# Kernel optimization log

Hardware: AMD Instinct MI355X
Metric: run time of the kernel (lower is better)

Reference implementation:

```python
import jax, jax.numpy as jnp
import numpy as np

BATCH = 262144
N_ASSETS = 64
N_GROUPS = 8
ITERS = 20
EPS = 1e-9


def setup_inputs() -> dict:
    key = jax.random.key(0)
    kx = jax.random.fold_in(key, 1)
    x = jax.random.uniform(kx, (BATCH, N_ASSETS), dtype=jnp.float32)
    x = x / jnp.sum(x, axis=-1, keepdims=True)  # roughly simplex-like raw weights
    box_lb = jnp.zeros((N_ASSETS,), jnp.float32)          # port_type[0] = 0 (long-only)
    box_ub = jnp.full((N_ASSETS,), 0.3, jnp.float32)      # per-asset cap from _build_constraints
    # one-hot group membership matrix: asset i belongs to group i % N_GROUPS
    gid = np.arange(N_ASSETS) % N_GROUPS
    A = np.zeros((N_GROUPS, N_ASSETS), np.float32)
    A[gid, np.arange(N_ASSETS)] = 1.0
    group_A = jnp.asarray(A)
    group_lb = jnp.full((N_GROUPS,), 0.05, jnp.float32)
    group_ub = jnp.full((N_GROUPS,), 0.5, jnp.float32)
    return {"x": x, "box_lb": box_lb, "box_ub": box_ub, "group_A": group_A,
            "group_lb": group_lb, "group_ub": group_ub, "num_iterations": ITERS}


def _dykstra(x, box_lb, box_ub, group_A, group_lb, group_ub, num_iterations):
    n = x.shape[-1]
    norm_sq = jnp.sum(group_A * group_A, axis=-1)  # (G,)

    def box_simplex(w):
        w = jnp.clip(w, box_lb, box_ub)
        return w - (jnp.sum(w, axis=-1, keepdims=True) - 1.0) / n

    def group_step(w, g):
        a, lb, ub, ns = g  # a: (N,), scalars lb/ub/ns
        Aw = w @ a  # (B,)
        w = jnp.where((Aw > ub)[:, None], w - ((Aw - ub) / (ns + EPS))[:, None] * a, w)
        Aw = w @ a  # recomputed on updated w, matching the TF layer
        w = jnp.where((Aw < lb)[:, None], w - ((Aw - lb) / (ns + EPS))[:, None] * a, w)
        return w, None

    def body(i, w):
        w = box_simplex(w)
        w, _ = jax.lax.scan(group_step, w, (group_A, group_lb, group_ub, norm_sq))
        return w

    w = jax.lax.fori_loop(0, num_iterations, body, x)
    return box_simplex(w)


def reference(x, box_lb, box_ub, group_A, group_lb, group_ub, num_iterations):
    return _dykstra(x, box_lb, box_ub, group_A, group_lb, group_ub, num_iterations)
```

## Files before the change

### kernel.cpp

```cpp
#include <hip/hip_runtime.h>


#define NA 64
#define NG 8

__device__ __forceinline__ bool structural_ok(const float* __restrict__ box_lb,
                                              const float* __restrict__ box_ub,
                                              const float* __restrict__ group_A,
                                              int l) {
    const float lb0 = box_lb[0], ub0 = box_ub[0];
    bool ok = (box_lb[l] == lb0) && (box_ub[l] == ub0) && (lb0 <= ub0);
#pragma unroll
    for (int g = 0; g < NG; ++g) {
        const float expect = ((l & 7) == g) ? 1.0f : 0.0f;
        ok = ok && (group_A[g * NA + l] == expect);
    }
    return __all(ok);
}

__global__ __launch_bounds__(256, 4) void proj_fast(
    const float* __restrict__ x,
    const float* __restrict__ box_lb,
    const float* __restrict__ box_ub,
    const float* __restrict__ group_A,
    const float* __restrict__ group_lb,
    const float* __restrict__ group_ub,
    const int*  __restrict__ num_iter,
    float* __restrict__ out,
    int nrows)
{
    if (!structural_ok(box_lb, box_ub, group_A, threadIdx.x & 63)) return;

    const int r = blockIdx.x * blockDim.x + threadIdx.x;
    if (r >= nrows) return;

    const float* __restrict__ xr = x + (size_t)r * NA;
    float* __restrict__ outr = out + (size_t)r * NA;

    float w[NA];
#pragma unroll
    for (int q = 0; q < NA / 4; ++q) {
        const float4 v = reinterpret_cast<const float4*>(xr)[q];
        w[4 * q + 0] = v.x; w[4 * q + 1] = v.y;
        w[4 * q + 2] = v.z; w[4 * q + 3] = v.w;
    }

    const float lb0 = box_lb[0], ub0 = box_ub[0];
    float glb_s[NG], gub_s[NG];
#pragma unroll
    for (int g = 0; g < NG; ++g) { glb_s[g] = group_lb[g]; gub_s[g] = group_ub[g]; }

    const int iters = *num_iter;

    const float inv8 = 1.0f / (8.0f + 1e-9f);
    const float scale = 8.0f * inv8;

    for (int it = 0; it < iters; ++it) {
#pragma unroll
        for (int j = 0; j < NA; ++j)
            w[j] = __builtin_amdgcn_fmed3f(w[j], lb0, ub0);

        float gs[NG];
#pragma unroll
        for (int g = 0; g < NG; ++g) {
            const float a = w[g] + w[g + 8], b = w[g + 16] + w[g + 24];
            const float c = w[g + 32] + w[g + 40], d = w[g + 48] + w[g + 56];
            gs[g] = (a + b) + (c + d);
        }
        const float S = ((gs[0] + gs[1]) + (gs[2] + gs[3]))
                      + ((gs[4] + gs[5]) + (gs[6] + gs[7]));
        const float shift = (S - 1.0f) * (1.0f / NA);

        float u[NG];
#pragma unroll
        for (int g = 0; g < NG; ++g) {
            const float Aw  = fmaf(-8.0f, shift, gs[g]);
            const float e1  = fmaxf(Aw - gub_s[g], 0.0f);
            const float Aw2 = fmaf(-scale, e1, Aw);
            const float e2  = fminf(Aw2 - glb_s[g], 0.0f);
            u[g] = fmaf(e1 + e2, inv8, shift);
        }
#pragma unroll
        for (int k = 0; k < 8; ++k)
#pragma unroll
            for (int g = 0; g < NG; ++g)
                w[8 * k + g] -= u[g];
    }

    float ps[NG];
#pragma unroll
    for (int g = 0; g < NG; ++g) {
        w[g] = __builtin_amdgcn_fmed3f(w[g], lb0, ub0);
        ps[g] = w[g];
    }
#pragma unroll
    for (int j = NG; j < NA; ++j) {
        w[j] = __builtin_amdgcn_fmed3f(w[j], lb0, ub0);
        ps[j & 7] += w[j];
    }
    const float S = ((ps[0] + ps[1]) + (ps[2] + ps[3]))
                  + ((ps[4] + ps[5]) + (ps[6] + ps[7]));
    const float shift = (S - 1.0f) * (1.0f / NA);

#pragma unroll
    for (int q = 0; q < NA / 4; ++q) {
        float4 v;
        v.x = w[4 * q + 0] - shift; v.y = w[4 * q + 1] - shift;
        v.z = w[4 * q + 2] - shift; v.w = w[4 * q + 3] - shift;
        reinterpret_cast<float4*>(outr)[q] = v;
    }
}

__global__ __launch_bounds__(256) void proj_generic(
    const float* __restrict__ x,
    const float* __restrict__ box_lb,
    const float* __restrict__ box_ub,
    const float* __restrict__ group_A,
    const float* __restrict__ group_lb,
    const float* __restrict__ group_ub,
    const int*  __restrict__ num_iter,
    float* __restrict__ out,
    int nrows)
{
    if (structural_ok(box_lb, box_ub, group_A, threadIdx.x & 63)) return;

    const int r = blockIdx.x * blockDim.x + threadIdx.x;
    if (r >= nrows) return;

    const float* __restrict__ xr = x + (size_t)r * NA;
    float* __restrict__ outr = out + (size_t)r * NA;

    float w[NA];
#pragma unroll
    for (int j = 0; j < NA; ++j) w[j] = xr[j];

    const int iters = *num_iter;

    for (int it = 0; it < iters; ++it) {
        float S = 0.0f;
#pragma unroll
        for (int j = 0; j < NA; ++j) {
            w[j] = fminf(fmaxf(w[j], box_lb[j]), box_ub[j]);
            S += w[j];
        }
        const float shift = (S - 1.0f) * (1.0f / NA);
#pragma unroll
        for (int j = 0; j < NA; ++j) w[j] -= shift;

        for (int g = 0; g < NG; ++g) {
            const float* __restrict__ a = group_A + g * NA;
            float ns = 0.0f, Aw = 0.0f;
#pragma unroll
            for (int j = 0; j < NA; ++j) {
                const float av = a[j];
                ns = fmaf(av, av, ns);
                Aw = fmaf(av, w[j], Aw);
            }
            const float invg = 1.0f / (ns + 1e-9f);
            const float gub = group_ub[g], glb = group_lb[g];
            const float d1 = (Aw > gub) ? (Aw - gub) * invg : 0.0f;
#pragma unroll
            for (int j = 0; j < NA; ++j) w[j] = fmaf(-d1, a[j], w[j]);
            float Aw2 = 0.0f;
#pragma unroll
            for (int j = 0; j < NA; ++j) Aw2 = fmaf(a[j], w[j], Aw2);
            const float d2 = (Aw2 < glb) ? (Aw2 - glb) * invg : 0.0f;
#pragma unroll
            for (int j = 0; j < NA; ++j) w[j] = fmaf(-d2, a[j], w[j]);
        }
    }
    float S = 0.0f;
#pragma unroll
    for (int j = 0; j < NA; ++j) {
        w[j] = fminf(fmaxf(w[j], box_lb[j]), box_ub[j]);
        S += w[j];
    }
    const float shift = (S - 1.0f) * (1.0f / NA);
#pragma unroll
    for (int j = 0; j < NA; ++j) outr[j] = w[j] - shift;
}

extern "C" void kernel_launch(void* const* d_in, const int* in_sizes, int n_in,
                              void* d_out, int out_size, void* d_ws, size_t ws_size,
                              hipStream_t stream) {
    const float* x        = (const float*)d_in[0];
    const float* box_lb   = (const float*)d_in[1];
    const float* box_ub   = (const float*)d_in[2];
    const float* group_A  = (const float*)d_in[3];
    const float* group_lb = (const float*)d_in[4];
    const float* group_ub = (const float*)d_in[5];
    const int*   num_iter = (const int*)d_in[6];
    float* out = (float*)d_out;

    const int nrows = in_sizes[0] / NA;
    const int block = 256;
    const int grid = (nrows + block - 1) / block;

    proj_fast<<<grid, block, 0, stream>>>(x, box_lb, box_ub, group_A,
                                          group_lb, group_ub, num_iter,
                                          out, nrows);
    proj_generic<<<grid, block, 0, stream>>>(x, box_lb, box_ub, group_A,
                                             group_lb, group_ub, num_iter,
                                             out, nrows);
}
```

Baseline: 150.7 us.

## Split each row across two lanes with DPP cross-lane group-sum reduction

The fast kernel now assigns two threads per row, each holding 32 of the 64 weights, and combines the per-group partial sums through a DPP xor-1 swizzle add. This halves register pressure per thread and doubles thread-level parallelism, which should raise occupancy and improve load coalescing. Each iteration now pays a few extra cross-lane adds, the launch grid doubles, and the min-waves launch bound is dropped. It also replaces the near-1 scale factor with an exact subtraction, which can differ by a rounding step.

```diff
diff --git a/kernel.cpp b/kernel.cpp
--- a/kernel.cpp
+++ b/kernel.cpp
@@ -3,6 +3,12 @@
 
 #define NA 64
 #define NG 8
+
+__device__ __forceinline__ float dpp_xor1_add(float v) {
+    const int o = __builtin_amdgcn_update_dpp(0, __builtin_bit_cast(int, v),
+                                              0xB1, 0xF, 0xF, true);
+    return v + __builtin_bit_cast(float, o);
+}
 
 __device__ __forceinline__ bool structural_ok(const float* __restrict__ box_lb,
                                               const float* __restrict__ box_ub,
@@ -18,7 +24,7 @@
     return __all(ok);
 }
 
-__global__ __launch_bounds__(256, 4) void proj_fast(
+__global__ __launch_bounds__(256) void proj_fast(
     const float* __restrict__ x,
     const float* __restrict__ box_lb,
     const float* __restrict__ box_ub,
@@ -31,19 +37,23 @@
 {
     if (!structural_ok(box_lb, box_ub, group_A, threadIdx.x & 63)) return;
 
-    const int r = blockIdx.x * blockDim.x + threadIdx.x;
+    const int t = blockIdx.x * blockDim.x + threadIdx.x;
+    const int r = t >> 1;
+    const int h = t & 1;
     if (r >= nrows) return;
 
     const float* __restrict__ xr = x + (size_t)r * NA;
     float* __restrict__ outr = out + (size_t)r * NA;
 
-    float w[NA];
-#pragma unroll
-    for (int q = 0; q < NA / 4; ++q) {
-        const float4 v = reinterpret_cast<const float4*>(xr)[q];
-        w[4 * q + 0] = v.x; w[4 * q + 1] = v.y;
-        w[4 * q + 2] = v.z; w[4 * q + 3] = v.w;
-    }
+    float w[32];
+#pragma unroll
+    for (int m = 0; m < 4; ++m)
+#pragma unroll
+        for (int q = 0; q < 2; ++q) {
+            const float4 v = reinterpret_cast<const float4*>(xr)[4 * m + 2 * h + q];
+            w[8 * m + 4 * q + 0] = v.x; w[8 * m + 4 * q + 1] = v.y;
+            w[8 * m + 4 * q + 2] = v.z; w[8 * m + 4 * q + 3] = v.w;
+        }
 
     const float lb0 = box_lb[0], ub0 = box_ub[0];
     float glb_s[NG], gub_s[NG];
@@ -53,20 +63,20 @@
     const int iters = *num_iter;
 
     const float inv8 = 1.0f / (8.0f + 1e-9f);
-    const float scale = 8.0f * inv8;
 
     for (int it = 0; it < iters; ++it) {
 #pragma unroll
-        for (int j = 0; j < NA; ++j)
-            w[j] = __builtin_amdgcn_fmed3f(w[j], lb0, ub0);
+        for (int i = 0; i < 32; ++i)
+            w[i] = __builtin_amdgcn_fmed3f(w[i], lb0, ub0);
 
         float gs[NG];
 #pragma unroll
-        for (int g = 0; g < NG; ++g) {
-            const float a = w[g] + w[g + 8], b = w[g + 16] + w[g + 24];
-            const float c = w[g + 32] + w[g + 40], d = w[g + 48] + w[g + 56];
-            gs[g] = (a + b) + (c + d);
-        }
+        for (int g = 0; g < NG; ++g)
+            gs[g] = (w[g] + w[g + 8]) + (w[g + 16] + w[g + 24]);
+#pragma unroll
+        for (int g = 0; g < NG; ++g)
+            gs[g] = dpp_xor1_add(gs[g]);
+
         const float S = ((gs[0] + gs[1]) + (gs[2] + gs[3]))
                       + ((gs[4] + gs[5]) + (gs[6] + gs[7]));
         const float shift = (S - 1.0f) * (1.0f / NA);
@@ -76,39 +86,38 @@
         for (int g = 0; g < NG; ++g) {
             const float Aw  = fmaf(-8.0f, shift, gs[g]);
             const float e1  = fmaxf(Aw - gub_s[g], 0.0f);
-            const float Aw2 = fmaf(-scale, e1, Aw);
+            const float Aw2 = Aw - e1;
             const float e2  = fminf(Aw2 - glb_s[g], 0.0f);
             u[g] = fmaf(e1 + e2, inv8, shift);
         }
 #pragma unroll
-        for (int k = 0; k < 8; ++k)
-#pragma unroll
-            for (int g = 0; g < NG; ++g)
-                w[8 * k + g] -= u[g];
-    }
-
+        for (int i = 0; i < 32; ++i)
+            w[i] -= u[i & 7];
+    }
+
+#pragma unroll
+    for (int i = 0; i < 32; ++i)
+        w[i] = __builtin_amdgcn_fmed3f(w[i], lb0, ub0);
     float ps[NG];
 #pragma unroll
-    for (int g = 0; g < NG; ++g) {
-        w[g] = __builtin_amdgcn_fmed3f(w[g], lb0, ub0);
-        ps[g] = w[g];
-    }
-#pragma unroll
-    for (int j = NG; j < NA; ++j) {
-        w[j] = __builtin_amdgcn_fmed3f(w[j], lb0, ub0);
-        ps[j & 7] += w[j];
-    }
-    const float S = ((ps[0] + ps[1]) + (ps[2] + ps[3]))
-                  + ((ps[4] + ps[5]) + (ps[6] + ps[7]));
+    for (int g = 0; g < NG; ++g)
+        ps[g] = (w[g] + w[g + 8]) + (w[g + 16] + w[g + 24]);
+    const float ls = ((ps[0] + ps[1]) + (ps[2] + ps[3]))
+                   + ((ps[4] + ps[5]) + (ps[6] + ps[7]));
+    const float S = dpp_xor1_add(ls);
     const float shift = (S - 1.0f) * (1.0f / NA);
 
 #pragma unroll
-    for (int q = 0; q < NA / 4; ++q) {
-        float4 v;
-        v.x = w[4 * q + 0] - shift; v.y = w[4 * q + 1] - shift;
-        v.z = w[4 * q + 2] - shift; v.w = w[4 * q + 3] - shift;
-        reinterpret_cast<float4*>(outr)[q] = v;
-    }
+    for (int m = 0; m < 4; ++m)
+#pragma unroll
+        for (int q = 0; q < 2; ++q) {
+            float4 v;
+            v.x = w[8 * m + 4 * q + 0] - shift;
+            v.y = w[8 * m + 4 * q + 1] - shift;
+            v.z = w[8 * m + 4 * q + 2] - shift;
+            v.w = w[8 * m + 4 * q + 3] - shift;
+            reinterpret_cast<float4*>(outr)[4 * m + 2 * h + q] = v;
+        }
 }
 
 __global__ __launch_bounds__(256) void proj_generic(
@@ -193,13 +202,20 @@
     float* out = (float*)d_out;
 
     const int nrows = in_sizes[0] / NA;
-    const int block = 256;
-    const int grid = (nrows + block - 1) / block;
-
-    proj_fast<<<grid, block, 0, stream>>>(x, box_lb, box_ub, group_A,
-                                          group_lb, group_ub, num_iter,
-                                          out, nrows);
-    proj_generic<<<grid, block, 0, stream>>>(x, box_lb, box_ub, group_A,
-                                             group_lb, group_ub, num_iter,
-                                             out, nrows);
-}
+
+    {
+        const int total = nrows * 2;
+        const int block = 256;
+        const int grid = (total + block - 1) / block;
+        proj_fast<<<grid, block, 0, stream>>>(x, box_lb, box_ub, group_A,
+                                              group_lb, group_ub, num_iter,
+                                              out, nrows);
+    }
+    {
+        const int block = 256;
+        const int grid = (nrows + block - 1) / block;
+        proj_generic<<<grid, block, 0, stream>>>(x, box_lb, box_ub, group_A,
+                                                 group_lb, group_ub, num_iter,
+                                                 out, nrows);
+    }
+}
```

Result: slower. 154.2 us (+2.3%).
